# Optimization experiments

Measured on AMD Instinct MI355X. Metric: run time of the kernel, lower is better.

## Reference

```python
import jax, jax.numpy as jnp
import numpy as np

N, M, E, F = 100000, 20000, 1000000, 128
LEAKY_SLOPE = 0.2
BN_EPS = 1e-5


def segment_softmax(logits, seg, num_segments):
    # numerically stable softmax over ragged segments
    mx = jax.ops.segment_max(logits, seg, num_segments=num_segments)
    mx = jnp.where(jnp.isfinite(mx), mx, 0.0)  # empty segments -> -inf -> 0
    e = jnp.exp(logits - mx[seg])
    s = jax.ops.segment_sum(e, seg, num_segments=num_segments)
    return e / (s[seg] + 1e-16)


def setup_inputs() -> dict:
    key = jax.random.key(0)
    ks = jax.random.split(key, 6)
    return {
        "x": jax.random.normal(ks[0], (N, F), jnp.float32),
        "hyperedge_attr": jax.random.normal(ks[1], (M, F), jnp.float32),
        "W": jax.random.normal(ks[2], (F, F), jnp.float32) / np.sqrt(F),
        "att": jax.random.normal(ks[3], (2 * F,), jnp.float32) * 0.1,
        "bias": jnp.zeros((F,), jnp.float32),
        "gamma": jnp.ones((F,), jnp.float32),
        "beta": jnp.zeros((F,), jnp.float32),
        "node_idx": jax.random.randint(ks[4], (E,), 0, N, dtype=jnp.int32),
        "edge_idx": jax.random.randint(ks[5], (E,), 0, M, dtype=jnp.int32),
    }


def reference(x, hyperedge_attr, W, att, bias, gamma, beta, node_idx, edge_idx):
    # --- HypergraphConv(use_attention=True, heads=1, attention_mode='node') ---
    xw = x @ W                     # [N, F] transformed node features
    ea = hyperedge_attr @ W        # [M, F] transformed hyperedge features (shared lin)

    # per-incidence attention logits: (cat[x_i, e_j] * att).sum(-1)
    a_node = xw @ att[:F]          # [N]
    a_edge = ea @ att[F:]          # [M]
    alpha = a_node[node_idx] + a_edge[edge_idx]          # [E]
    alpha = jax.nn.leaky_relu(alpha, LEAKY_SLOPE)
    alpha = segment_softmax(alpha, edge_idx, M)          # softmax per hyperedge

    ones = jnp.ones((E,), xw.dtype)
    D = jax.ops.segment_sum(ones, node_idx, num_segments=N)   # node degree
    Dinv = jnp.where(D > 0, 1.0 / D, 0.0)
    Bdeg = jax.ops.segment_sum(ones, edge_idx, num_segments=M)  # hyperedge size
    Binv = jnp.where(Bdeg > 0, 1.0 / Bdeg, 0.0)

    # node -> hyperedge: gather node feats, weight by B^{-1}*alpha, scatter to edges
    m1 = (Binv[edge_idx] * alpha)[:, None] * xw[node_idx]        # [E, F]
    edge_feat = jax.ops.segment_sum(m1, edge_idx, num_segments=M)  # [M, F]

    # hyperedge -> node: gather edge feats, weight by D^{-1}*alpha, scatter to nodes
    m2 = (Dinv[node_idx] * alpha)[:, None] * edge_feat[edge_idx]  # [E, F]
    out = jax.ops.segment_sum(m2, node_idx, num_segments=N) + bias  # [N, F]

    # --- BatchNorm1d (training-mode batch statistics, biased variance) ---
    mu = out.mean(axis=0)
    var = out.var(axis=0)
    out = gamma * (out - mu) * jax.lax.rsqrt(var + BN_EPS) + beta

    # --- ELU, dropout (eval: identity), residual (in_dim == out_dim) ---
    out = jax.nn.elu(out)
    return out + x
```

## Files before the change

### kernel.cpp

```cpp
#include <hip/hip_runtime.h>
#include <hip/hip_bf16.h>

#define NN 100000
#define MM 20000
#define EE 1000000
#define FF 128

#define EBK 157
#define NBK 782
#define ECAP 7168
#define NCAP 1664
#define CHUNK 2048
#define NREP 64

typedef unsigned short u16;
typedef unsigned int u32;
typedef __attribute__((ext_vector_type(8))) short short8v;
typedef __attribute__((ext_vector_type(4))) float f32x4;

__device__ __forceinline__ u16 f2bf(float f) {
  u32 x = __float_as_uint(f);
  return (u16)((x + 0x7FFFu + ((x >> 16) & 1u)) >> 16);
}
__device__ __forceinline__ float bf2f(u16 u) { return __uint_as_float(((u32)u) << 16); }
__device__ __forceinline__ float leaky(float v) { return v > 0.f ? v : 0.2f * v; }
__device__ __forceinline__ float readlane_f(float v, int l) {
  return __uint_as_float((u32)__builtin_amdgcn_readlane((int)__float_as_uint(v), l));
}

__global__ __launch_bounds__(256) void k_prep(const float* __restrict__ W,
                                              const float* __restrict__ att,
                                              float* __restrict__ watt2, u16* __restrict__ WtSwz,
                                              int* __restrict__ ecur, int* __restrict__ ncur,
                                              float* __restrict__ bn_partial) {
  int gid = blockIdx.x * 256 + threadIdx.x;
  if (gid < EBK) ecur[gid] = 0;
  if (gid < NBK) ncur[gid] = 0;
  if (gid < NREP * 256) bn_partial[gid] = 0.f;
  if (blockIdx.x == 0 && threadIdx.x < 128) {
    int t = threadIdx.x;
    float s2 = 0.f;
    for (int c = 0; c < FF; c += 4) {
      float4 wv = *(const float4*)(W + t * FF + c);
      s2 += wv.x * att[FF + c] + wv.y * att[FF + c + 1] + wv.z * att[FF + c + 2] + wv.w * att[FF + c + 3];
    }
    watt2[t] = s2;
    int c = t;
    for (int k = 0; k < FF; k += 2) {
      u32 p = (u32)f2bf(W[k * FF + c]) | ((u32)f2bf(W[(k + 1) * FF + c]) << 16);
      int byte = c * 256 + ((k * 2) ^ ((c & 7) << 4));
      *(u32*)((char*)WtSwz + byte) = p;
    }
  }
}

__global__ __launch_bounds__(256) void k_gemm(const float* __restrict__ x,
                                              const u16* __restrict__ WtSwz,
                                              const float* __restrict__ att,
                                              u16* __restrict__ xw,
                                              float* __restrict__ a_node) {
  __shared__ u16 Wl[FF * FF];
  __shared__ u16 xl[64 * FF];
  int t = threadIdx.x;
  {
    const uint4* src = (const uint4*)WtSwz;
    uint4* dst = (uint4*)Wl;
    for (int i = t; i < FF * FF * 2 / 16; i += 256) dst[i] = src[i];
  }
  int row0 = blockIdx.x * 64;
  for (int chunk = t; chunk < 64 * 32; chunk += 256) {
    int r = chunk >> 5;
    int j = chunk & 31;
    float4 v = make_float4(0.f, 0.f, 0.f, 0.f);
    if (row0 + r < NN) v = ((const float4*)(x + (size_t)(row0 + r) * FF))[j];
    uint2 p;
    p.x = (u32)f2bf(v.x) | ((u32)f2bf(v.y) << 16);
    p.y = (u32)f2bf(v.z) | ((u32)f2bf(v.w) << 16);
    int byte = r * 256 + ((j * 8) ^ ((r & 7) << 4));
    *(uint2*)((char*)xl + byte) = p;
  }
  __syncthreads();

  int wid = t >> 6, lane = t & 63;
  int r_lo = lane & 15, khalf = lane >> 4;
  f32x4 acc[8];
#pragma unroll
  for (int ct = 0; ct < 8; ++ct) acc[ct] = (f32x4){0.f, 0.f, 0.f, 0.f};

#pragma unroll
  for (int kc = 0; kc < 4; ++kc) {
    int kbyte = kc * 64 + khalf * 16;
    int arow = wid * 16 + r_lo;
    short8v a = *(const short8v*)((const char*)xl + arow * 256 + (kbyte ^ ((arow & 7) << 4)));
#pragma unroll
    for (int ct = 0; ct < 8; ++ct) {
      int brow = ct * 16 + r_lo;
      short8v b = *(const short8v*)((const char*)Wl + brow * 256 + (kbyte ^ ((brow & 7) << 4)));
      acc[ct] = __builtin_amdgcn_mfma_f32_16x16x32_bf16(a, b, acc[ct], 0, 0, 0);
    }
  }

  float att_c[8];
#pragma unroll
  for (int ct = 0; ct < 8; ++ct) att_c[ct] = att[ct * 16 + r_lo];
  float p[4] = {0.f, 0.f, 0.f, 0.f};
#pragma unroll
  for (int ct = 0; ct < 8; ++ct) {
#pragma unroll
    for (int reg = 0; reg < 4; ++reg) {
      int lrow = wid * 16 + khalf * 4 + reg;
      int grow = row0 + lrow;
      if (grow < NN) xw[(size_t)grow * FF + ct * 16 + r_lo] = f2bf(acc[ct][reg]);
      p[reg] += acc[ct][reg] * att_c[ct];
    }
  }
#pragma unroll
  for (int off = 1; off <= 8; off <<= 1) {
#pragma unroll
    for (int reg = 0; reg < 4; ++reg) p[reg] += __shfl_xor(p[reg], off, 64);
  }
  if (r_lo == 0) {
#pragma unroll
    for (int reg = 0; reg < 4; ++reg) {
      int grow = row0 + wid * 16 + khalf * 4 + reg;
      if (grow < NN) a_node[grow] = p[reg];
    }
  }
}

__global__ __launch_bounds__(256) void k_aedge(const float* __restrict__ he,
                                               const float* __restrict__ watt2,
                                               float* __restrict__ a_edge) {
  int m = (blockIdx.x * 256 + threadIdx.x) >> 6;
  int lane = threadIdx.x & 63;
  if (m >= MM) return;
  float2 wv = ((const float2*)watt2)[lane];
  float2 v = ((const float2*)(he + (size_t)m * FF))[lane];
  float p = v.x * wv.x + v.y * wv.y;
#pragma unroll
  for (int off = 32; off; off >>= 1) p += __shfl_xor(p, off, 64);
  if (lane == 0) a_edge[m] = p;
}

__global__ __launch_bounds__(256) void k_binA(const int* __restrict__ node_idx,
                                              const int* __restrict__ edge_idx,
                                              int* __restrict__ ecur, int* __restrict__ ncur,
                                              u32* __restrict__ ebins, u32* __restrict__ nbins) {
  __shared__ int ecnt[EBK], ncnt[NBK], ebase[EBK], nbase[NBK];
  int t = threadIdx.x;
  for (int i = t; i < EBK; i += 256) ecnt[i] = 0;
  for (int i = t; i < NBK; i += 256) ncnt[i] = 0;
  __syncthreads();
  int start = blockIdx.x * CHUNK;
  int end = min(start + CHUNK, EE);
  for (int e = start + t; e < end; e += 256) {
    int m = edge_idx[e], n = node_idx[e];
    atomicAdd(&ecnt[m >> 7], 1);
    atomicAdd(&ncnt[n >> 7], 1);
  }
  __syncthreads();
  for (int i = t; i < EBK; i += 256) {
    int c = ecnt[i];
    ebase[i] = c ? atomicAdd(&ecur[i], c) : 0;
    ecnt[i] = 0;
  }
  for (int i = t; i < NBK; i += 256) {
    int c = ncnt[i];
    nbase[i] = c ? atomicAdd(&ncur[i], c) : 0;
    ncnt[i] = 0;
  }
  __syncthreads();
  for (int e = start + t; e < end; e += 256) {
    int m = edge_idx[e], n = node_idx[e];
    int eb = m >> 7, nb = n >> 7;
    int p = ebase[eb] + atomicAdd(&ecnt[eb], 1);
    if (p < ECAP) ebins[eb * ECAP + p] = ((u32)n << 7) | (u32)(m & 127);
    int q = nbase[nb] + atomicAdd(&ncnt[nb], 1);
    if (q < NCAP) nbins[nb * NCAP + q] = ((u32)m << 7) | (u32)(n & 127);
  }
}

__global__ __launch_bounds__(1024) void k_bscan2(const int* __restrict__ ecur, int* __restrict__ ebot,
                                                 const int* __restrict__ ncur, int* __restrict__ nbot) {
  __shared__ int sd[1024];
  const int* cur = blockIdx.x == 0 ? ecur : ncur;
  int* bot = blockIdx.x == 0 ? ebot : nbot;
  int len = blockIdx.x == 0 ? EBK : NBK;
  int t = threadIdx.x;
  int v = (t < len) ? cur[t] : 0;
  sd[t] = v;
  __syncthreads();
  for (int off = 1; off < 1024; off <<= 1) {
    int u = (t >= off) ? sd[t - off] : 0;
    __syncthreads();
    sd[t] += u;
    __syncthreads();
  }
  if (t < len) bot[t] = sd[t] - v;
}

__global__ __launch_bounds__(256) void k_binB(const u32* __restrict__ ebins,
                                              const int* __restrict__ ecur,
                                              const int* __restrict__ ebot,
                                              int* __restrict__ edge_ptr,
                                              int* __restrict__ csrE_node,
                                              const u32* __restrict__ nbins,
                                              const int* __restrict__ ncur,
                                              const int* __restrict__ nbot,
                                              int* __restrict__ node_ptr,
                                              int* __restrict__ csrN_edge) {
  __shared__ int cnt[128], cur[128], sc[128];
  int t = threadIdx.x;
  bool is_edge = blockIdx.x < EBK;
  int b = is_edge ? blockIdx.x : blockIdx.x - EBK;
  const u32* src = is_edge ? (ebins + (size_t)b * ECAP) : (nbins + (size_t)b * NCAP);
  int count = is_edge ? min(ecur[b], ECAP) : min(ncur[b], NCAP);
  int gbase = is_edge ? ebot[b] : nbot[b];
  int* ptr = is_edge ? edge_ptr : node_ptr;
  int* csr = is_edge ? csrE_node : csrN_edge;
  int glen = is_edge ? MM : NN;
  int nbk = is_edge ? EBK : NBK;
  if (t < 128) cnt[t] = 0;
  __syncthreads();
  for (int i = t; i < count; i += 256) atomicAdd(&cnt[src[i] & 127], 1);
  __syncthreads();
  if (t < 128) sc[t] = cnt[t];
  __syncthreads();
  for (int off = 1; off < 128; off <<= 1) {
    int u = (t >= off && t < 128) ? sc[t - off] : 0;
    __syncthreads();
    if (t < 128) sc[t] += u;
    __syncthreads();
  }
  if (t < 128) {
    int excl = sc[t] - cnt[t];
    cur[t] = excl;
    int g = b * 128 + t;
    if (g < glen) ptr[g] = gbase + excl;
  }
  if (b == nbk - 1 && t == 0) ptr[glen] = gbase + count;
  __syncthreads();
  for (int i = t; i < count; i += 256) {
    u32 v = src[i];
    int pos = atomicAdd(&cur[v & 127], 1);
    csr[gbase + pos] = (int)(v >> 7);
  }
}

__global__ __launch_bounds__(256) void k_edge_agg(const int* __restrict__ edge_ptr,
                                                  const int* __restrict__ csrE_node,
                                                  const float* __restrict__ a_node,
                                                  const float* __restrict__ a_edge,
                                                  const u16* __restrict__ xw,
                                                  u16* __restrict__ edge_feat,
                                                  float4* __restrict__ edge_sc) {
  int m = (blockIdx.x * 256 + threadIdx.x) >> 6;
  int lane = threadIdx.x & 63;
  if (m >= MM) return;
  int s0 = edge_ptr[m], s1 = edge_ptr[m + 1];
  int len = s1 - s0;
  if (len == 0) return;
  float ae = a_edge[m];

  float lm = -1e30f, ls = 0.f, v0 = -1e30f;
  int n0 = 0;
  for (int base = s0; base < s1; base += 64) {
    int i = base + lane;
    if (i < s1) {
      int n = csrE_node[i];
      float v = leaky(a_node[n] + ae);
      if (base == s0) { v0 = v; n0 = n; }
      float mnew = fmaxf(lm, v);
      ls = ls * __expf(lm - mnew) + __expf(v - mnew);
      lm = mnew;
    }
  }
#pragma unroll
  for (int off = 1; off < 64; off <<= 1) {
    float m2 = __shfl_xor(lm, off, 64);
    float s2 = __shfl_xor(ls, off, 64);
    float mnew = fmaxf(lm, m2);
    ls = ls * __expf(lm - mnew) + s2 * __expf(m2 - mnew);
    lm = mnew;
  }
  float mxv = lm;
  float invs = 1.0f / (ls + 1e-16f);

  float accx = 0.f, accy = 0.f;
  for (int base = s0; base < s1; base += 64) {
    int i = base + lane;
    bool valid = i < s1;
    int n_l;
    float w_l;
    if (base == s0) {
      n_l = n0;
      w_l = valid ? __expf(v0 - mxv) : 0.f;
    } else {
      n_l = valid ? csrE_node[i] : 0;
      w_l = valid ? __expf(leaky(a_node[n_l] + ae) - mxv) : 0.f;
    }
    int cnt = min(64, s1 - base);
    for (int b = 0; b < cnt; b += 16) {
      u32 u[16];
      float wv[16];
#pragma unroll
      for (int j = 0; j < 16; ++j) {
        int n = __builtin_amdgcn_readlane(n_l, b + j);
        wv[j] = readlane_f(w_l, b + j);
        u[j] = *(const u32*)(xw + (size_t)n * FF + 2 * lane);
      }
#pragma unroll
      for (int j = 0; j < 16; ++j) {
        accx += wv[j] * bf2f((u16)u[j]);
        accy += wv[j] * bf2f((u16)(u[j] >> 16));
      }
    }
  }
  float r = invs / (float)len;
  u32 packed = (u32)f2bf(accx * r) | ((u32)f2bf(accy * r) << 16);
  *(u32*)(edge_feat + (size_t)m * FF + 2 * lane) = packed;
  if (lane == 0) edge_sc[m] = make_float4(ae, mxv, invs, 0.f);
}

__global__ __launch_bounds__(256) void k_node_agg(const int* __restrict__ node_ptr,
                                                  const int* __restrict__ csrN_edge,
                                                  const float* __restrict__ a_node,
                                                  const u16* __restrict__ edge_feat,
                                                  const float4* __restrict__ edge_sc,
                                                  const float* __restrict__ bias,
                                                  float* __restrict__ out,
                                                  float* __restrict__ bn_partial) {
  __shared__ float4 sd[4][64];
  int wid = threadIdx.x >> 6, lane = threadIdx.x & 63;
  float2 bv = ((const float2*)bias)[lane];
  float s1x = 0.f, s1y = 0.f, s2x = 0.f, s2y = 0.f;
#pragma unroll
  for (int k = 0; k < 2; ++k) {
    int n = blockIdx.x * 8 + wid * 2 + k;
    if (n >= NN) break;
    int s0 = node_ptr[n], s1 = node_ptr[n + 1];
    float an = a_node[n];
    float accx = 0.f, accy = 0.f;
    for (int base = s0; base < s1; base += 64) {
      int i = base + lane;
      bool valid = i < s1;
      int m_l = valid ? csrN_edge[i] : 0;
      float w_l = 0.f;
      if (valid) {
        float4 sc = edge_sc[m_l];
        w_l = __expf(leaky(an + sc.x) - sc.y) * sc.z;
      }
      int cnt = min(64, s1 - base);
      for (int b = 0; b < cnt; b += 16) {
        u32 u[16];
        float wv[16];
#pragma unroll
        for (int j = 0; j < 16; ++j) {
          int mm = __builtin_amdgcn_readlane(m_l, b + j);
          wv[j] = readlane_f(w_l, b + j);
          u[j] = *(const u32*)(edge_feat + (size_t)mm * FF + 2 * lane);
        }
#pragma unroll
        for (int j = 0; j < 16; ++j) {
          accx += wv[j] * bf2f((u16)u[j]);
          accy += wv[j] * bf2f((u16)(u[j] >> 16));
        }
      }
    }
    int deg = s1 - s0;
    float dinv = deg > 0 ? 1.0f / (float)deg : 0.f;
    float2 o;
    o.x = accx * dinv + bv.x;
    o.y = accy * dinv + bv.y;
    ((float2*)(out + (size_t)n * FF))[lane] = o;
    s1x += o.x; s1y += o.y;
    s2x += o.x * o.x; s2y += o.y * o.y;
  }
  sd[wid][lane] = make_float4(s1x, s1y, s2x, s2y);
  __syncthreads();
  if (wid == 0) {
    float4 a0 = sd[0][lane], a1 = sd[1][lane], a2 = sd[2][lane], a3 = sd[3][lane];
    float4 s;
    s.x = a0.x + a1.x + a2.x + a3.x;
    s.y = a0.y + a1.y + a2.y + a3.y;
    s.z = a0.z + a1.z + a2.z + a3.z;
    s.w = a0.w + a1.w + a2.w + a3.w;
    float* bp = bn_partial + (blockIdx.x & (NREP - 1)) * 256;
    atomicAdd(bp + 2 * lane, s.x);
    atomicAdd(bp + 2 * lane + 1, s.y);
    atomicAdd(bp + 128 + 2 * lane, s.z);
    atomicAdd(bp + 128 + 2 * lane + 1, s.w);
  }
}

__global__ void k_bn_final(const float* __restrict__ bn_partial, const float* __restrict__ gamma,
                           const float* __restrict__ beta, float* __restrict__ ss) {
  int c = threadIdx.x;
  float s1 = 0.f, s2 = 0.f;
  for (int r = 0; r < NREP; ++r) {
    s1 += bn_partial[r * 256 + c];
    s2 += bn_partial[r * 256 + 128 + c];
  }
  float mu = s1 * (1.0f / NN);
  float var = s2 * (1.0f / NN) - mu * mu;
  var = fmaxf(var, 0.f);
  float sc = gamma[c] * rsqrtf(var + 1e-5f);
  ss[c] = sc;
  ss[FF + c] = beta[c] - mu * sc;
}

__global__ __launch_bounds__(256) void k_finalize(float* __restrict__ out,
                                                  const float* __restrict__ x,
                                                  const float* __restrict__ ss) {
  int idx = blockIdx.x * 256 + threadIdx.x;
  float4 v = ((const float4*)out)[idx];
  float4 xr = ((const float4*)x)[idx];
  int cb = (idx * 4) & 127;
  float4 sc = *(const float4*)(ss + cb);
  float4 sh = *(const float4*)(ss + FF + cb);
  v.x = fmaf(v.x, sc.x, sh.x);
  v.y = fmaf(v.y, sc.y, sh.y);
  v.z = fmaf(v.z, sc.z, sh.z);
  v.w = fmaf(v.w, sc.w, sh.w);
  v.x = v.x > 0.f ? v.x : expm1f(v.x);
  v.y = v.y > 0.f ? v.y : expm1f(v.y);
  v.z = v.z > 0.f ? v.z : expm1f(v.z);
  v.w = v.w > 0.f ? v.w : expm1f(v.w);
  v.x += xr.x; v.y += xr.y; v.z += xr.z; v.w += xr.w;
  ((float4*)out)[idx] = v;
}

extern "C" void kernel_launch(void* const* d_in, const int* in_sizes, int n_in,
                              void* d_out, int out_size, void* d_ws, size_t ws_size,
                              hipStream_t stream) {
  const float* x     = (const float*)d_in[0];
  const float* he    = (const float*)d_in[1];
  const float* W     = (const float*)d_in[2];
  const float* att   = (const float*)d_in[3];
  const float* bias  = (const float*)d_in[4];
  const float* gamma = (const float*)d_in[5];
  const float* beta  = (const float*)d_in[6];
  const int* node_idx = (const int*)d_in[7];
  const int* edge_idx = (const int*)d_in[8];
  float* out = (float*)d_out;

  char* w = (char*)d_ws;
  auto alloc = [&](size_t bytes) -> char* {
    char* p = w;
    w += (bytes + 255) & ~(size_t)255;
    return p;
  };
  u16*   xw        = (u16*)  alloc((size_t)NN * FF * 2);
  float* a_node    = (float*)alloc((size_t)NN * 4);
  float* a_edge    = (float*)alloc((size_t)MM * 4);
  u16*   WtSwz     = (u16*)  alloc((size_t)FF * FF * 2);
  float* watt2     = (float*)alloc(FF * 4);
  u16*   edge_feat = (u16*)  alloc((size_t)MM * FF * 2);
  float4* edge_sc  = (float4*)alloc((size_t)MM * 16);
  int* edge_ptr    = (int*)  alloc((size_t)(MM + 1) * 4);
  int* node_ptr    = (int*)  alloc((size_t)(NN + 1) * 4);
  int* csrE_node   = (int*)  alloc((size_t)EE * 4);
  int* csrN_edge   = (int*)  alloc((size_t)EE * 4);
  int* ecur        = (int*)  alloc((size_t)EBK * 4);
  int* ncur        = (int*)  alloc((size_t)NBK * 4);
  int* ebot        = (int*)  alloc((size_t)EBK * 4);
  int* nbot        = (int*)  alloc((size_t)NBK * 4);
  u32* ebins       = (u32*)  alloc((size_t)EBK * ECAP * 4);
  u32* nbins       = (u32*)  alloc((size_t)NBK * NCAP * 4);
  float* bn_partial= (float*)alloc((size_t)NREP * 256 * 4);
  float* ss        = (float*)alloc(2 * FF * 4);

  k_prep<<<64, 256, 0, stream>>>(W, att, watt2, WtSwz, ecur, ncur, bn_partial);
  k_gemm<<<(NN + 63) / 64, 256, 0, stream>>>(x, WtSwz, att, xw, a_node);
  k_aedge<<<(MM * 64 + 255) / 256, 256, 0, stream>>>(he, watt2, a_edge);

  k_binA<<<(EE + CHUNK - 1) / CHUNK, 256, 0, stream>>>(node_idx, edge_idx, ecur, ncur, ebins, nbins);
  k_bscan2<<<2, 1024, 0, stream>>>(ecur, ebot, ncur, nbot);
  k_binB<<<EBK + NBK, 256, 0, stream>>>(ebins, ecur, ebot, edge_ptr, csrE_node,
                                        nbins, ncur, nbot, node_ptr, csrN_edge);

  k_edge_agg<<<(MM + 3) / 4, 256, 0, stream>>>(edge_ptr, csrE_node, a_node, a_edge, xw, edge_feat, edge_sc);
  k_node_agg<<<(NN + 7) / 8, 256, 0, stream>>>(node_ptr, csrN_edge, a_node, edge_feat, edge_sc, bias, out, bn_partial);
  k_bn_final<<<1, 128, 0, stream>>>(bn_partial, gamma, beta, ss);
  k_finalize<<<(NN * FF / 4 + 255) / 256, 256, 0, stream>>>(out, x, ss);
}
```

Before: 214.0 us.

## Simplify binning to global atomics, store pre-BN output in bf16, widen node blocks

The shared-memory two-pass binning kernel is replaced by one thread per incidence that takes a slot with a global atomic on the bin cursor. The node aggregation kernel now handles 16 nodes per block instead of 8. It writes the pre-BatchNorm output as bf16 into a new workspace buffer when the workspace is large enough, and the finalize kernel reads that buffer back. This halves the bytes of the intermediate write and read, at the cost of bf16 rounding before normalization and far more contention on the global atomics. The NN bounds check is dropped, which is safe only because NN is a multiple of 16.

```diff
diff --git a/kernel.cpp b/kernel.cpp
--- a/kernel.cpp
+++ b/kernel.cpp
@@ -10,7 +10,6 @@
 #define NBK 782
 #define ECAP 7168
 #define NCAP 1664
-#define CHUNK 2048
 #define NREP 64
 
 typedef unsigned short u16;
@@ -146,38 +145,14 @@
                                               const int* __restrict__ edge_idx,
                                               int* __restrict__ ecur, int* __restrict__ ncur,
                                               u32* __restrict__ ebins, u32* __restrict__ nbins) {
-  __shared__ int ecnt[EBK], ncnt[NBK], ebase[EBK], nbase[NBK];
-  int t = threadIdx.x;
-  for (int i = t; i < EBK; i += 256) ecnt[i] = 0;
-  for (int i = t; i < NBK; i += 256) ncnt[i] = 0;
-  __syncthreads();
-  int start = blockIdx.x * CHUNK;
-  int end = min(start + CHUNK, EE);
-  for (int e = start + t; e < end; e += 256) {
-    int m = edge_idx[e], n = node_idx[e];
-    atomicAdd(&ecnt[m >> 7], 1);
-    atomicAdd(&ncnt[n >> 7], 1);
-  }
-  __syncthreads();
-  for (int i = t; i < EBK; i += 256) {
-    int c = ecnt[i];
-    ebase[i] = c ? atomicAdd(&ecur[i], c) : 0;
-    ecnt[i] = 0;
-  }
-  for (int i = t; i < NBK; i += 256) {
-    int c = ncnt[i];
-    nbase[i] = c ? atomicAdd(&ncur[i], c) : 0;
-    ncnt[i] = 0;
-  }
-  __syncthreads();
-  for (int e = start + t; e < end; e += 256) {
-    int m = edge_idx[e], n = node_idx[e];
-    int eb = m >> 7, nb = n >> 7;
-    int p = ebase[eb] + atomicAdd(&ecnt[eb], 1);
-    if (p < ECAP) ebins[eb * ECAP + p] = ((u32)n << 7) | (u32)(m & 127);
-    int q = nbase[nb] + atomicAdd(&ncnt[nb], 1);
-    if (q < NCAP) nbins[nb * NCAP + q] = ((u32)m << 7) | (u32)(n & 127);
-  }
+  int e = blockIdx.x * 256 + threadIdx.x;
+  if (e >= EE) return;
+  int m = edge_idx[e], n = node_idx[e];
+  int eb = m >> 7, nb = n >> 7;
+  int p = atomicAdd(&ecur[eb], 1);
+  if (p < ECAP) ebins[(size_t)eb * ECAP + p] = ((u32)n << 7) | (u32)(m & 127);
+  int q = atomicAdd(&ncur[nb], 1);
+  if (q < NCAP) nbins[(size_t)nb * NCAP + q] = ((u32)m << 7) | (u32)(n & 127);
 }
 
 __global__ __launch_bounds__(1024) void k_bscan2(const int* __restrict__ ecur, int* __restrict__ ebot,
@@ -328,16 +303,16 @@
                                                   const u16* __restrict__ edge_feat,
                                                   const float4* __restrict__ edge_sc,
                                                   const float* __restrict__ bias,
-                                                  float* __restrict__ out,
+                                                  float* __restrict__ out_f32,
+                                                  u16* __restrict__ raw_bf,
                                                   float* __restrict__ bn_partial) {
   __shared__ float4 sd[4][64];
   int wid = threadIdx.x >> 6, lane = threadIdx.x & 63;
   float2 bv = ((const float2*)bias)[lane];
   float s1x = 0.f, s1y = 0.f, s2x = 0.f, s2y = 0.f;
 #pragma unroll
-  for (int k = 0; k < 2; ++k) {
-    int n = blockIdx.x * 8 + wid * 2 + k;
-    if (n >= NN) break;
+  for (int k = 0; k < 4; ++k) {
+    int n = blockIdx.x * 16 + wid * 4 + k;
     int s0 = node_ptr[n], s1 = node_ptr[n + 1];
     float an = a_node[n];
     float accx = 0.f, accy = 0.f;
@@ -369,12 +344,15 @@
     }
     int deg = s1 - s0;
     float dinv = deg > 0 ? 1.0f / (float)deg : 0.f;
-    float2 o;
-    o.x = accx * dinv + bv.x;
-    o.y = accy * dinv + bv.y;
-    ((float2*)(out + (size_t)n * FF))[lane] = o;
-    s1x += o.x; s1y += o.y;
-    s2x += o.x * o.x; s2y += o.y * o.y;
+    float ox = accx * dinv + bv.x;
+    float oy = accy * dinv + bv.y;
+    if (raw_bf) {
+      *(u32*)(raw_bf + (size_t)n * FF + 2 * lane) = (u32)f2bf(ox) | ((u32)f2bf(oy) << 16);
+    } else {
+      ((float2*)(out_f32 + (size_t)n * FF))[lane] = make_float2(ox, oy);
+    }
+    s1x += ox; s1y += oy;
+    s2x += ox * ox; s2y += oy * oy;
   }
   sd[wid][lane] = make_float4(s1x, s1y, s2x, s2y);
   __syncthreads();
@@ -410,10 +388,17 @@
 }
 
 __global__ __launch_bounds__(256) void k_finalize(float* __restrict__ out,
+                                                  const u16* __restrict__ raw_bf,
                                                   const float* __restrict__ x,
                                                   const float* __restrict__ ss) {
   int idx = blockIdx.x * 256 + threadIdx.x;
-  float4 v = ((const float4*)out)[idx];
+  float4 v;
+  if (raw_bf) {
+    ushort4 rv = *(const ushort4*)(raw_bf + (size_t)idx * 4);
+    v = make_float4(bf2f(rv.x), bf2f(rv.y), bf2f(rv.z), bf2f(rv.w));
+  } else {
+    v = ((const float4*)out)[idx];
+  }
   float4 xr = ((const float4*)x)[idx];
   int cb = (idx * 4) & 127;
   float4 sc = *(const float4*)(ss + cb);
@@ -469,18 +454,21 @@
   u32* nbins       = (u32*)  alloc((size_t)NBK * NCAP * 4);
   float* bn_partial= (float*)alloc((size_t)NREP * 256 * 4);
   float* ss        = (float*)alloc(2 * FF * 4);
+  u16*   raw_cand  = (u16*)  alloc((size_t)NN * FF * 2);
+  size_t need = (size_t)(w - (char*)d_ws);
+  u16* raw_bf = (need <= ws_size) ? raw_cand : (u16*)nullptr;
 
   k_prep<<<64, 256, 0, stream>>>(W, att, watt2, WtSwz, ecur, ncur, bn_partial);
   k_gemm<<<(NN + 63) / 64, 256, 0, stream>>>(x, WtSwz, att, xw, a_node);
   k_aedge<<<(MM * 64 + 255) / 256, 256, 0, stream>>>(he, watt2, a_edge);
 
-  k_binA<<<(EE + CHUNK - 1) / CHUNK, 256, 0, stream>>>(node_idx, edge_idx, ecur, ncur, ebins, nbins);
+  k_binA<<<(EE + 255) / 256, 256, 0, stream>>>(node_idx, edge_idx, ecur, ncur, ebins, nbins);
   k_bscan2<<<2, 1024, 0, stream>>>(ecur, ebot, ncur, nbot);
   k_binB<<<EBK + NBK, 256, 0, stream>>>(ebins, ecur, ebot, edge_ptr, csrE_node,
                                         nbins, ncur, nbot, node_ptr, csrN_edge);
 
   k_edge_agg<<<(MM + 3) / 4, 256, 0, stream>>>(edge_ptr, csrE_node, a_node, a_edge, xw, edge_feat, edge_sc);
-  k_node_agg<<<(NN + 7) / 8, 256, 0, stream>>>(node_ptr, csrN_edge, a_node, edge_feat, edge_sc, bias, out, bn_partial);
+  k_node_agg<<<NN / 16, 256, 0, stream>>>(node_ptr, csrN_edge, a_node, edge_feat, edge_sc, bias, out, raw_bf, bn_partial);
   k_bn_final<<<1, 128, 0, stream>>>(bn_partial, gamma, beta, ss);
-  k_finalize<<<(NN * FF / 4 + 255) / 256, 256, 0, stream>>>(out, x, ss);
-}
+  k_finalize<<<(NN * FF / 4 + 255) / 256, 256, 0, stream>>>(out, raw_bf, x, ss);
+}
```

Result: slower. 852.7 us (+298.6%).
